# Optimization experiments

Measured on AMD Instinct MI355X. Metric: run time of the kernel, lower is better.

The kernel has to match this reference:

```python
import jax, jax.numpy as jnp
import numpy as np


def reference(x, phi, sigma, M_phi_plus, M_phi_minus, M_u, padded_sl):
    """STU forward: spectral FFT convolution + autoregressive input term.

    x:   (B, L, D) input sequence
    phi: (L, K) time-domain spectral filters (top-K Hankel eigenvectors);
         V = rfft(phi, n=padded_sl) matches the module's precomputed V.
    sigma: (K,) Hankel eigenvalues
    M_phi_plus/minus: (K, D, D) per-filter projections
    M_u: (k_u, D, D) AR-on-input matrices
    """
    B, L, D = x.shape
    K = sigma.shape[0]
    n = padded_sl  # FFT length for causal linear convolution

    # Alternating-sign trick for the 'minus' featurization:
    # sum_j (-1)^j phi_j u_{t-j} = (-1)^t * conv(phi, sgn*u)_t
    sgn = jnp.where(jnp.arange(L) % 2 == 0, 1.0, -1.0).astype(x.dtype)[None, :, None]  # (1,L,1)

    V = jnp.fft.rfft(phi, n=n, axis=0)                       # (n//2+1, K) complex
    U = jnp.fft.rfft(jnp.stack([x, x * sgn], axis=-1), n=n, axis=1)  # (B, n//2+1, D, 2)
    prod = V[None, :, :, None, None] * U[:, :, None, :, :]    # (B, n//2+1, K, D, 2)
    conv = jnp.fft.irfft(prod, n=n, axis=1)[:, :L]            # (B, L, K, D, 2) causal conv
    U_plus = conv[..., 0]
    U_minus = conv[..., 1] * sgn[..., None]                   # undo sign on output side

    # Fold sigma^{1/4} scaling into the projection matrices.
    sig4 = (sigma ** 0.25).astype(x.dtype)[:, None, None]     # (K,1,1)
    spectral = (
        jnp.einsum('blkd,kdo->blo', U_plus, M_phi_plus * sig4)
        + jnp.einsum('blkd,kdo->blo', U_minus, M_phi_minus * sig4)
    )

    # compute_ar_u: y_t += sum_{i=0}^{k_u-1} x_{t-i} @ M_u[i]  (use_ar_u=True)
    ar_u = jnp.einsum('bld,do->blo', x, M_u[0])
    for i in range(1, M_u.shape[0]):  # small fixed depth k_u=3
        x_shift = jnp.pad(x, ((0, 0), (i, 0), (0, 0)))[:, :L]
        ar_u = ar_u + jnp.einsum('bld,do->blo', x_shift, M_u[i])

    # use_ar_y=False branch; dropout=0 (identity)
    return spectral + ar_u


def setup_inputs() -> dict:
    key = jax.random.key(0)
    ks = jax.random.split(key, 6)
    B, L, D, K, KU, N = 1, 2048, 768, 16, 3, 4096
    x = jax.random.normal(ks[0], (B, L, D), jnp.float32)
    phi = jax.random.normal(ks[1], (L, K), jnp.float32) / np.sqrt(L).astype(np.float32)
    sigma = jax.random.uniform(ks[2], (K,), jnp.float32, 0.1, 1.0)
    M_phi_plus = jax.random.normal(ks[3], (K, D, D), jnp.float32) * 0.02
    M_phi_minus = jax.random.normal(ks[4], (K, D, D), jnp.float32) * 0.02
    M_u = jax.random.normal(ks[5], (KU, D, D), jnp.float32) * 0.02
    return {"x": x, "phi": phi, "sigma": sigma, "M_phi_plus": M_phi_plus,
            "M_phi_minus": M_phi_minus, "M_u": M_u, "padded_sl": N}
```

## Files before the change

### kernel.cpp

```cpp
#include <hip/hip_runtime.h>

typedef __attribute__((ext_vector_type(8))) short bf16x8;
typedef __attribute__((ext_vector_type(4))) float f32x4;

#define SL 2048
#define DM 768
#define NCH 32
#define MSPEC 24576
#define MTOT  26880

__device__ __forceinline__ short f2bf(float f) {
  unsigned u = __builtin_bit_cast(unsigned, f);
  u = (u + 0x7FFFu + ((u >> 16) & 1u)) >> 16;
  return (short)u;
}

__device__ __forceinline__ void gload16(const short* g, short* l) {
  __builtin_amdgcn_global_load_lds(
      (const __attribute__((address_space(1))) void*)g,
      (__attribute__((address_space(3))) void*)l, 16, 0, 0);
}


__global__ __launch_bounds__(256) void k_zero(float4* out) {
  out[blockIdx.x * 256 + threadIdx.x] = float4{0.f, 0.f, 0.f, 0.f};
}

__global__ __launch_bounds__(256) void k_prep_xT(const float* __restrict__ x,
                                                 short* __restrict__ xT) {
  __shared__ short tile[64][65];
  const int d0 = blockIdx.x * 64, l0 = blockIdx.y * 64;
  const int t = threadIdx.x;
#pragma unroll
  for (int rr = 0; rr < 16; ++rr) {
    int ll = rr * 4 + (t >> 6), dl = t & 63;
    tile[ll][dl] = f2bf(x[(size_t)(l0 + ll) * DM + d0 + dl]);
  }
  __syncthreads();
#pragma unroll
  for (int rr = 0; rr < 16; ++rr) {
    int dl = rr * 4 + (t >> 6), ll = t & 63;
    xT[(size_t)(d0 + dl) * SL + l0 + ll] = tile[ll][dl];
  }
}

__global__ __launch_bounds__(256) void k_prep_ar(const float* __restrict__ x,
                                                 short* __restrict__ U) {
  int id = blockIdx.x * 256 + threadIdx.x;
  int l = id / DM, d = id - l * DM;
#pragma unroll
  for (int i = 0; i < 3; ++i) {
    short v = 0;
    if (l >= i) v = f2bf(x[(size_t)(l - i) * DM + d]);
    U[(size_t)l * MTOT + MSPEC + i * DM + d] = v;
  }
}

__global__ __launch_bounds__(256) void k_prep_T(const float* __restrict__ phi,
                                                short* __restrict__ Tmat) {
  int idx = blockIdx.x * 256 + threadIdx.x;
  int b = idx & 127, a = (idx >> 7) & 127, dlag = (idx >> 14) & 15, c = idx >> 18;
  int j = dlag * 128 + a - b;
  short v = 0;
  if (j >= 0) {
    float p = phi[j * 16 + (c & 15)];
    if (c >= 16 && (j & 1)) p = -p;
    v = f2bf(p);
  }
  Tmat[idx] = v;
}

__global__ __launch_bounds__(256) void k_prep_M(const float* __restrict__ Mp,
                                                const float* __restrict__ Mm,
                                                const float* __restrict__ Mu,
                                                const float* __restrict__ sigma,
                                                short* __restrict__ McatT) {
  __shared__ short tile[64][65];
  const int m0 = blockIdx.x * 64, o0 = blockIdx.y * 64;
  const int t = threadIdx.x;
#pragma unroll
  for (int rr = 0; rr < 16; ++rr) {
    int ml = rr * 4 + (t >> 6), ol = t & 63;
    int m = m0 + ml, o = o0 + ol;
    float v;
    if (m < MSPEC) {
      int c = m / DM, d = m - c * DM;
      int k = c & 15;
      float s4 = sqrtf(sqrtf(sigma[k]));
      if (c < 16) v = Mp[((size_t)c * DM + d) * DM + o] * s4;
      else        v = Mm[((size_t)(c - 16) * DM + d) * DM + o] * s4;
    } else {
      int mm = m - MSPEC;
      int i = mm / DM, d = mm - i * DM;
      v = Mu[((size_t)i * DM + d) * DM + o];
    }
    tile[ml][ol] = f2bf(v);
  }
  __syncthreads();
#pragma unroll
  for (int rr = 0; rr < 16; ++rr) {
    int ol = rr * 4 + (t >> 6), ml = t & 63;
    McatT[(size_t)(o0 + ol) * MTOT + m0 + ml] = tile[ml][ol];
  }
}

__global__ __launch_bounds__(256) void k_gemm1(const short* __restrict__ Tmat,
                                               const short* __restrict__ xT,
                                               short* __restrict__ U) {
  __shared__ __align__(16) short As[2][128 * 32];
  __shared__ __align__(16) short Bs[2][128 * 32];
  const int wid = blockIdx.x;
  const int xcd = wid & 7;
  const int slot = wid >> 3;
  const int c = xcd * 4 + (slot & 3);
  const int dtile = (slot >> 2) % 6;
  const int ib = 15 - (slot >> 2) / 6;
  const int t = threadIdx.x;
  const int lane = t & 63, wave = t >> 6;
  const int wm = (wave >> 1) * 64, wn = (wave & 1) * 64;
  const int lrow = lane & 15, quad = lane >> 4;
  const int l4 = lane >> 2, lq = lane & 3;
  const int r0 = wave * 32 + l4;
  const int swz = (lq ^ ((l4 >> 1) & 3)) * 8;
  const int foff = ((quad ^ ((lrow >> 1) & 3)) << 3);

  f32x4 acc[4][4] = {};
  const short* Abase = Tmat + ((size_t)(c * 16) << 14) + r0 * 128 + swz;
  const short* Bbase = xT + (size_t)dtile * 128 * SL + (size_t)r0 * SL + swz;
  const int nit = 4 * (ib + 1);

  auto stage = [&](int it, int buf) {
    int dlag = it >> 2, kk = it & 3;
    const short* Ad = Abase + ((size_t)dlag << 14) + kk * 32;
    const short* Bd = Bbase + (ib - dlag) * 128 + kk * 32;
    short* lA = &As[buf][wave * 1024 + lane * 8];
    short* lB = &Bs[buf][wave * 1024 + lane * 8];
    gload16(Ad, lA);
    gload16(Ad + 16 * 128, lA + 512);
    gload16(Bd, lB);
    gload16(Bd + 16 * SL, lB + 512);
  };

  stage(0, 0);
  int cur = 0;
  for (int it = 0; it < nit; ++it) {
    __syncthreads();
    if (it + 1 < nit) stage(it + 1, cur ^ 1);
    bf16x8 af[4], bfr[4];
#pragma unroll
    for (int im = 0; im < 4; ++im)
      af[im] = *reinterpret_cast<const bf16x8*>(&As[cur][(wm + im * 16 + lrow) * 32 + foff]);
#pragma unroll
    for (int in = 0; in < 4; ++in)
      bfr[in] = *reinterpret_cast<const bf16x8*>(&Bs[cur][(wn + in * 16 + lrow) * 32 + foff]);
#pragma unroll
    for (int im = 0; im < 4; ++im)
#pragma unroll
      for (int in = 0; in < 4; ++in)
        acc[im][in] = __builtin_amdgcn_mfma_f32_16x16x32_bf16(af[im], bfr[in], acc[im][in], 0, 0, 0);
    cur ^= 1;
  }
  const int l0 = ib * 128, colbase = c * DM + dtile * 128;
#pragma unroll
  for (int im = 0; im < 4; ++im)
#pragma unroll
    for (int in = 0; in < 4; ++in)
#pragma unroll
      for (int r4 = 0; r4 < 4; ++r4) {
        int row = wm + im * 16 + quad * 4 + r4;
        int col = wn + in * 16 + lrow;
        U[(size_t)(l0 + row) * MTOT + colbase + col] = f2bf(acc[im][in][r4]);
      }
}

__global__ __launch_bounds__(256) void k_gemm2(const short* __restrict__ U,
                                               const short* __restrict__ McatT,
                                               float* __restrict__ out) {
  __shared__ __align__(16) short As[2][128 * 32];
  __shared__ __align__(16) short Bs[2][128 * 32];
  const int wid = blockIdx.x;
  const int kc = wid & 7;
  const int slot = wid >> 3;
  const int otile = slot % 6;
  const int lb = slot / 6;
  const int t = threadIdx.x;
  const int lane = t & 63, wave = t >> 6;
  const int wm = (wave >> 1) * 64, wn = (wave & 1) * 64;
  const int lrow = lane & 15, quad = lane >> 4;
  const int l4 = lane >> 2, lq = lane & 3;
  const int r0 = wave * 32 + l4;
  const int swz = (lq ^ ((l4 >> 1) & 3)) * 8;
  const int foff = ((quad ^ ((lrow >> 1) & 3)) << 3);

  f32x4 acc[4][4] = {};
  const short* Ab = U + (size_t)lb * 128 * MTOT + kc * 3360 + (size_t)r0 * MTOT + swz;
  const short* Bb = McatT + (size_t)otile * 128 * MTOT + kc * 3360 + (size_t)r0 * MTOT + swz;

  auto stage = [&](int s, int buf) {
    short* lA = &As[buf][wave * 1024 + lane * 8];
    short* lB = &Bs[buf][wave * 1024 + lane * 8];
    gload16(Ab + s * 32, lA);
    gload16(Ab + s * 32 + (size_t)16 * MTOT, lA + 512);
    gload16(Bb + s * 32, lB);
    gload16(Bb + s * 32 + (size_t)16 * MTOT, lB + 512);
  };

  stage(0, 0);
  int cur = 0;
  for (int s = 0; s < 105; ++s) {
    __syncthreads();
    if (s + 1 < 105) stage(s + 1, cur ^ 1);
    bf16x8 af[4], bfr[4];
#pragma unroll
    for (int im = 0; im < 4; ++im)
      af[im] = *reinterpret_cast<const bf16x8*>(&As[cur][(wm + im * 16 + lrow) * 32 + foff]);
#pragma unroll
    for (int in = 0; in < 4; ++in)
      bfr[in] = *reinterpret_cast<const bf16x8*>(&Bs[cur][(wn + in * 16 + lrow) * 32 + foff]);
#pragma unroll
    for (int im = 0; im < 4; ++im)
#pragma unroll
      for (int in = 0; in < 4; ++in)
        acc[im][in] = __builtin_amdgcn_mfma_f32_16x16x32_bf16(af[im], bfr[in], acc[im][in], 0, 0, 0);
    cur ^= 1;
  }
  const int l0 = lb * 128, o0 = otile * 128;
#pragma unroll
  for (int im = 0; im < 4; ++im)
#pragma unroll
    for (int in = 0; in < 4; ++in)
#pragma unroll
      for (int r4 = 0; r4 < 4; ++r4) {
        int row = wm + im * 16 + quad * 4 + r4;
        int col = wn + in * 16 + lrow;
        atomicAdd(&out[(size_t)(l0 + row) * DM + o0 + col], acc[im][in][r4]);
      }
}

extern "C" void kernel_launch(void* const* d_in, const int* in_sizes, int n_in,
                              void* d_out, int out_size, void* d_ws, size_t ws_size,
                              hipStream_t stream) {
  (void)in_sizes; (void)n_in; (void)out_size; (void)ws_size;
  const float* x     = (const float*)d_in[0];
  const float* phi   = (const float*)d_in[1];
  const float* sigma = (const float*)d_in[2];
  const float* Mp    = (const float*)d_in[3];
  const float* Mm    = (const float*)d_in[4];
  const float* Mu    = (const float*)d_in[5];
  float* out = (float*)d_out;
  char* ws = (char*)d_ws;

  short* U     = (short*)(ws);
  short* Tmat  = (short*)(ws + 110100480);
  short* xT    = (short*)(ws + 126877696);
  short* McatT = (short*)(ws + 130023424);

  k_zero<<<dim3(1536), dim3(256), 0, stream>>>((float4*)out);
  k_prep_xT<<<dim3(12, 32), dim3(256), 0, stream>>>(x, xT);
  k_prep_ar<<<dim3(6144), dim3(256), 0, stream>>>(x, U);
  k_prep_T<<<dim3(32768), dim3(256), 0, stream>>>(phi, Tmat);
  k_prep_M<<<dim3(420, 12), dim3(256), 0, stream>>>(Mp, Mm, Mu, sigma, McatT);
  k_gemm1<<<dim3(3072), dim3(256), 0, stream>>>(Tmat, xT, U);
  k_gemm2<<<dim3(768), dim3(256), 0, stream>>>(U, McatT, out);
}
```

Measured before the change: 429.1 us.

## Rewrite second GEMM as 256x256 tiled 8-wave ping-pong pipeline with split-K 10

Replaces the 128x128 tile, 4-wave double-buffered GEMM2 with a 256x256 tile, 512-thread kernel. It uses split-K over 10 slices (240 blocks) and an eight-phase schedule that interleaves async global-to-LDS loads with MFMA bursts under explicit waitcnt, barriers and setprio. The aim is to raise data reuse per loaded tile and hide memory latency behind MFMA work. In exchange it uses more registers and LDS per block, hand-tuned waitcnt counts that must match the load issue order exactly, and possible imbalance from having only 240 blocks.

Result: faster. 419.5 us (-2.3%).

```diff
diff --git a/kernel.cpp b/kernel.cpp
--- a/kernel.cpp
+++ b/kernel.cpp
@@ -8,6 +8,11 @@
 #define NCH 32
 #define MSPEC 24576
 #define MTOT  26880
+
+#define SPLITK 10
+#define KSLICE 2688
+#define NT 42
+#define NITER 21
 
 __device__ __forceinline__ short f2bf(float f) {
   unsigned u = __builtin_bit_cast(unsigned, f);
@@ -173,67 +178,109 @@
       }
 }
 
-__global__ __launch_bounds__(256) void k_gemm2(const short* __restrict__ U,
-                                               const short* __restrict__ McatT,
-                                               float* __restrict__ out) {
-  __shared__ __align__(16) short As[2][128 * 32];
-  __shared__ __align__(16) short Bs[2][128 * 32];
-  const int wid = blockIdx.x;
-  const int kc = wid & 7;
-  const int slot = wid >> 3;
-  const int otile = slot % 6;
-  const int lb = slot / 6;
+
+#define LDSREADS(BUF, KS, MQ)                                                   \
+    _Pragma("unroll")                                                           \
+    for (int q_ = 0; q_ < 4; ++q_)                                              \
+      af_[q_] = *reinterpret_cast<const bf16x8*>(                               \
+          &As[BUF][KS][wm1][((MQ) * 64 + q_ * 16 + lrow) * 32 + foff]);         \
+    if ((MQ) == 0) {                                                            \
+      _Pragma("unroll")                                                         \
+      for (int i_ = 0; i_ < 4; ++i_)                                            \
+        bf_[i_] = *reinterpret_cast<const bf16x8*>(                             \
+            &Bs[BUF][KS][hB][(rB0 + i_ * 16 + lrow) * 32 + foff]);              \
+    }
+
+#define DOMFMA(MQ)                                                              \
+    _Pragma("unroll")                                                           \
+    for (int q_ = 0; q_ < 4; ++q_)                                              \
+      _Pragma("unroll")                                                         \
+      for (int i_ = 0; i_ < 4; ++i_)                                            \
+        acc[(MQ) * 4 + q_][i_] = __builtin_amdgcn_mfma_f32_16x16x32_bf16(       \
+            af_[q_], bf_[i_], acc[(MQ) * 4 + q_][i_], 0, 0, 0)
+
+#define STA(SBUF, SKS, SKT) do { int kt_ = (SKT); if (kt_ < NT) {               \
+    const short* g_ = Abase + kt_ * 64 + (SKS) * 32;                            \
+    gload16(g_, &As[SBUF][SKS][0][t8]);                                         \
+    gload16(g_ + (size_t)128 * MTOT, &As[SBUF][SKS][1][t8]); } } while (0)
+
+#define STB(SBUF, SKS, SKT) do { int kt_ = (SKT); if (kt_ < NT) {               \
+    const short* g_ = Bbase + kt_ * 64 + (SKS) * 32;                            \
+    gload16(g_, &Bs[SBUF][SKS][0][t8]);                                         \
+    gload16(g_ + (size_t)128 * MTOT, &Bs[SBUF][SKS][1][t8]); } } while (0)
+
+#define PHASE(BUF, KS, MQ, VMODE, STG) do {                                     \
+    asm volatile("" ::: "memory");            \
+    bf16x8 af_[4];                                                              \
+    if ((VMODE) == 1) asm volatile("s_waitcnt vmcnt(6)" ::: "memory");          \
+    if ((VMODE) == 2) {                                                         \
+      if (j < NITER - 1) asm volatile("s_waitcnt vmcnt(6)" ::: "memory");       \
+      else               asm volatile("s_waitcnt vmcnt(0)" ::: "memory");       \
+    }                                                                           \
+    if ((VMODE) == 0) { LDSREADS(BUF, KS, MQ) }                                 \
+    STG;                                                                        \
+    __builtin_amdgcn_s_barrier();                                               \
+    asm volatile("" ::: "memory");                                              \
+    if ((VMODE) != 0) { LDSREADS(BUF, KS, MQ) }                                 \
+    asm volatile("s_waitcnt lgkmcnt(0)" ::: "memory");                          \
+    __builtin_amdgcn_sched_barrier(0);                                          \
+    __builtin_amdgcn_s_setprio(1);                                              \
+    DOMFMA(MQ);                                                                 \
+    __builtin_amdgcn_s_setprio(0);                                              \
+    __builtin_amdgcn_s_barrier();                                               \
+  } while (0)
+
+__global__ __launch_bounds__(512, 2) void k_gemm2_8p(const short* __restrict__ U,
+                                                     const short* __restrict__ McatT,
+                                                     float* __restrict__ out) {
+  __shared__ __align__(16) short As[2][2][2][4096];
+  __shared__ __align__(16) short Bs[2][2][2][4096];
+  const int bid = blockIdx.x;
+  const int tile = bid % 24, kc = bid / 24;
+  const int mt = tile & 7, nt_ = tile >> 3;
+  const int m0 = mt * 256, o0 = nt_ * 256;
+  const int kbase = kc * KSLICE;
   const int t = threadIdx.x;
   const int lane = t & 63, wave = t >> 6;
-  const int wm = (wave >> 1) * 64, wn = (wave & 1) * 64;
+  const int wm1 = wave >> 2;
+  const int hB = (wave & 3) >> 1;
+  const int rB0 = (wave & 1) * 64;
   const int lrow = lane & 15, quad = lane >> 4;
-  const int l4 = lane >> 2, lq = lane & 3;
-  const int r0 = wave * 32 + l4;
-  const int swz = (lq ^ ((l4 >> 1) & 3)) * 8;
-  const int foff = ((quad ^ ((lrow >> 1) & 3)) << 3);
-
-  f32x4 acc[4][4] = {};
-  const short* Ab = U + (size_t)lb * 128 * MTOT + kc * 3360 + (size_t)r0 * MTOT + swz;
-  const short* Bb = McatT + (size_t)otile * 128 * MTOT + kc * 3360 + (size_t)r0 * MTOT + swz;
-
-  auto stage = [&](int s, int buf) {
-    short* lA = &As[buf][wave * 1024 + lane * 8];
-    short* lB = &Bs[buf][wave * 1024 + lane * 8];
-    gload16(Ab + s * 32, lA);
-    gload16(Ab + s * 32 + (size_t)16 * MTOT, lA + 512);
-    gload16(Bb + s * 32, lB);
-    gload16(Bb + s * 32 + (size_t)16 * MTOT, lB + 512);
-  };
-
-  stage(0, 0);
-  int cur = 0;
-  for (int s = 0; s < 105; ++s) {
-    __syncthreads();
-    if (s + 1 < 105) stage(s + 1, cur ^ 1);
-    bf16x8 af[4], bfr[4];
-#pragma unroll
-    for (int im = 0; im < 4; ++im)
-      af[im] = *reinterpret_cast<const bf16x8*>(&As[cur][(wm + im * 16 + lrow) * 32 + foff]);
+  const int foff = (quad ^ ((lrow >> 1) & 3)) << 3;
+  const int r = t >> 2;
+  const int cswz = ((t & 3) ^ ((r >> 1) & 3)) << 3;
+  const int t8 = t * 8;
+
+  const short* Abase = U     + (size_t)(m0 + r) * MTOT + kbase + cswz;
+  const short* Bbase = McatT + (size_t)(o0 + r) * MTOT + kbase + cswz;
+
+  f32x4 acc[8][4] = {};
+
+  STB(0, 0, 0); STA(0, 0, 0); STB(0, 1, 0); STA(0, 1, 0);
+  STB(1, 0, 1); STA(1, 0, 1); STB(1, 1, 1);
+
+  for (int j = 0; j < NITER; ++j) {
+    bf16x8 bf_[4];
+    PHASE(0, 0, 0, 1, STA(1, 1, 2 * j + 1));
+    PHASE(0, 0, 1, 0, STB(0, 0, 2 * j + 2));
+    PHASE(0, 1, 0, 0, STA(0, 0, 2 * j + 2));
+    PHASE(0, 1, 1, 0, STB(0, 1, 2 * j + 2));
+    PHASE(1, 0, 0, 2, STA(0, 1, 2 * j + 2));
+    PHASE(1, 0, 1, 0, STB(1, 0, 2 * j + 3));
+    PHASE(1, 1, 0, 0, STA(1, 0, 2 * j + 3));
+    PHASE(1, 1, 1, 0, STB(1, 1, 2 * j + 3));
+  }
+
+  const int wm128 = (wave >> 2) * 128, wn64 = (wave & 3) * 64;
+#pragma unroll
+  for (int im = 0; im < 8; ++im)
 #pragma unroll
     for (int in = 0; in < 4; ++in)
-      bfr[in] = *reinterpret_cast<const bf16x8*>(&Bs[cur][(wn + in * 16 + lrow) * 32 + foff]);
-#pragma unroll
-    for (int im = 0; im < 4; ++im)
-#pragma unroll
-      for (int in = 0; in < 4; ++in)
-        acc[im][in] = __builtin_amdgcn_mfma_f32_16x16x32_bf16(af[im], bfr[in], acc[im][in], 0, 0, 0);
-    cur ^= 1;
-  }
-  const int l0 = lb * 128, o0 = otile * 128;
-#pragma unroll
-  for (int im = 0; im < 4; ++im)
-#pragma unroll
-    for (int in = 0; in < 4; ++in)
 #pragma unroll
       for (int r4 = 0; r4 < 4; ++r4) {
-        int row = wm + im * 16 + quad * 4 + r4;
-        int col = wn + in * 16 + lrow;
-        atomicAdd(&out[(size_t)(l0 + row) * DM + o0 + col], acc[im][in][r4]);
+        int row = m0 + wm128 + im * 16 + quad * 4 + r4;
+        int col = o0 + wn64 + in * 16 + lrow;
+        atomicAdd(&out[(size_t)row * DM + col], acc[im][in][r4]);
       }
 }
 
@@ -261,5 +308,5 @@
   k_prep_T<<<dim3(32768), dim3(256), 0, stream>>>(phi, Tmat);
   k_prep_M<<<dim3(420, 12), dim3(256), 0, stream>>>(Mp, Mm, Mu, sigma, McatT);
   k_gemm1<<<dim3(3072), dim3(256), 0, stream>>>(Tmat, xT, U);
-  k_gemm2<<<dim3(768), dim3(256), 0, stream>>>(U, McatT, out);
-}
+  k_gemm2_8p<<<dim3(240), dim3(512), 0, stream>>>(U, McatT, out);
+}
```
